# Optimization experiments

Hardware: AMD Instinct MI355X
Metric: run time of the kernel (lower is better)

Reference implementation:

```python
import jax, jax.numpy as jnp
import numpy as np

DIM = 256
NUM_HEADS = 8
HEAD_DIM = DIM // NUM_HEADS
SCALE = 1.0 / DIM ** 0.5  # NOTE: source scales by 1/sqrt(dim), not 1/sqrt(head_dim)


def setup_inputs() -> dict:
    key = jax.random.key(0)
    k_x, k_wqkv, k_wout = jax.random.split(key, 3)
    x = jax.random.normal(k_x, (4, 2048, DIM), dtype=jnp.float32)
    # xavier_uniform for Linear(dim, 3*dim): limit = sqrt(6/(fan_in+fan_out))
    lim_qkv = float(np.sqrt(6.0 / (DIM + 3 * DIM)))
    w_qkv = jax.random.uniform(k_wqkv, (3 * DIM, DIM), minval=-lim_qkv, maxval=lim_qkv, dtype=jnp.float32)
    b_qkv = jnp.zeros((3 * DIM,), dtype=jnp.float32)
    lim_out = float(np.sqrt(6.0 / (DIM + DIM)))
    w_out = jax.random.uniform(k_wout, (DIM, DIM), minval=-lim_out, maxval=lim_out, dtype=jnp.float32)
    b_out = jnp.zeros((DIM,), dtype=jnp.float32)
    return {"x": x, "w_qkv": w_qkv, "b_qkv": b_qkv, "w_out": w_out, "b_out": b_out}


def reference(x, w_qkv, b_qkv, w_out, b_out):
    B, N, C = x.shape
    H, D = NUM_HEADS, C // NUM_HEADS
    qkv = x @ w_qkv.T + b_qkv                       # [B, N, 3C]
    qkv = qkv.reshape(B, N, 3, H, D)
    q = qkv[:, :, 0].transpose(0, 2, 1, 3)          # [B, H, N, D]
    k = qkv[:, :, 1].transpose(0, 2, 1, 3)
    v = qkv[:, :, 2].transpose(0, 2, 1, 3)
    attn = jnp.einsum("bhnd,bhmd->bhnm", q, k) * SCALE  # [B, H, N, N]
    attn = jax.nn.softmax(attn, axis=-1)
    z = jnp.einsum("bhnm,bhmd->bhnd", attn, v)      # [B, H, N, D]
    z = z.transpose(0, 2, 1, 3).reshape(B, N, C)
    return z @ w_out.T + b_out
```

## Files before the change

### kernel.cpp

```cpp
#include <hip/hip_runtime.h>


#define SEQ 2048
#define BATCH 4
#define NHEADS 8
#define HDIM 32
#define DIMC 256
#define SCALE_LOG2E 0.09016844005556021f

typedef __attribute__((ext_vector_type(8))) short short8;
typedef __attribute__((ext_vector_type(4))) float f32x4;

union BF8 { unsigned u[4]; short8 s8; };

__device__ __forceinline__ unsigned pk2bf(float a, float b) {
    union { float f; unsigned u; } ua, ub;
    ua.f = a; ub.f = b;
    return __builtin_amdgcn_perm(ub.u + 0x8000u, ua.u + 0x8000u, 0x07060302u);
}
__device__ __forceinline__ short f2bf(float a) {
    union { float f; unsigned u; } x; x.f = a;
    return (short)((x.u + 0x8000u) >> 16);
}

#define NX (BATCH * SEQ * DIMC)
#define NQW (3 * DIMC * DIMC)
#define NOW (DIMC * DIMC)

__global__ __launch_bounds__(256) void cvt_bf16(const float* __restrict__ x,
                                                const float* __restrict__ wq,
                                                const float* __restrict__ wo,
                                                short* __restrict__ xb,
                                                short* __restrict__ wqb,
                                                short* __restrict__ wob) {
    int i = (blockIdx.x * 256 + threadIdx.x) * 4;
    const float* src;
    short* dst;
    int off;
    if (i < NX) { src = x; dst = xb; off = i; }
    else if (i < NX + NQW) { src = wq; dst = wqb; off = i - NX; }
    else { src = wo; dst = wob; off = i - NX - NQW; }
    float4 v = *(const float4*)&src[off];
    uint2 p;
    p.x = pk2bf(v.x, v.y);
    p.y = pk2bf(v.z, v.w);
    *(uint2*)&dst[off] = p;
}

__global__ __launch_bounds__(256) void qkv_mfma(const short* __restrict__ Xb,
                                                const short* __restrict__ Wb,
                                                const float* __restrict__ bias,
                                                short* __restrict__ Q,
                                                short* __restrict__ Kd,
                                                short* __restrict__ V) {
    __shared__ __align__(16) union SM {
        struct { short A[128][72]; short B[64][72]; } ab;
        short CQ[128][72];
        short CV[64][136];
    } sm;

    const int m0 = blockIdx.y * 128, bx = blockIdx.x;
    const int n0 = bx * 64;
    const int tid = threadIdx.x;
    const int w = tid >> 6, lane = tid & 63;
    const int m = lane & 15, g = lane >> 4;
    const int wr = w >> 1, wc = w & 1;

    const int arow = tid >> 1, acol = (tid & 1) * 32;
    const int brow = tid >> 2, bcol = (tid & 3) * 16;

    f32x4 acc[4][2] = {};

    const short* ap = Xb + (size_t)(m0 + arow) * DIMC + acol;
    const short* bp = Wb + (size_t)(n0 + brow) * DIMC + bcol;

    short8 pa[4], pb[2];
#pragma unroll
    for (int i = 0; i < 4; i++) pa[i] = *(const short8*)(ap + i * 8);
#pragma unroll
    for (int i = 0; i < 2; i++) pb[i] = *(const short8*)(bp + i * 8);

    for (int kt = 0; kt < DIMC; kt += 64) {
        __syncthreads();
#pragma unroll
        for (int i = 0; i < 4; i++) *(short8*)&sm.ab.A[arow][acol + i * 8] = pa[i];
#pragma unroll
        for (int i = 0; i < 2; i++) *(short8*)&sm.ab.B[brow][bcol + i * 8] = pb[i];
        __syncthreads();
        if (kt + 64 < DIMC) {
#pragma unroll
            for (int i = 0; i < 4; i++) pa[i] = *(const short8*)(ap + kt + 64 + i * 8);
#pragma unroll
            for (int i = 0; i < 2; i++) pb[i] = *(const short8*)(bp + kt + 64 + i * 8);
        }
#pragma unroll
        for (int kk = 0; kk < 2; kk++) {
            short8 af[4], bf[2];
#pragma unroll
            for (int mt = 0; mt < 4; mt++)
                af[mt] = *(const short8*)&sm.ab.A[wr * 64 + mt * 16 + m][kk * 32 + g * 8];
#pragma unroll
            for (int nt = 0; nt < 2; nt++)
                bf[nt] = *(const short8*)&sm.ab.B[wc * 32 + nt * 16 + m][kk * 32 + g * 8];
#pragma unroll
            for (int mt = 0; mt < 4; mt++)
#pragma unroll
                for (int nt = 0; nt < 2; nt++)
                    acc[mt][nt] = __builtin_amdgcn_mfma_f32_16x16x32_bf16(af[mt], bf[nt], acc[mt][nt], 0, 0, 0);
        }
    }

    const int which = bx >> 2;
    const int h0 = (bx & 3) * 2;
    const int bidx = blockIdx.y >> 4;
    const int ntok0 = (blockIdx.y & 15) * 128;
    float bv[2];
#pragma unroll
    for (int nt = 0; nt < 2; nt++) bv[nt] = bias[n0 + wc * 32 + nt * 16 + m];

    __syncthreads();
    if (which != 2) {
        const float qs = (which == 0) ? SCALE_LOG2E : 1.0f;
#pragma unroll
        for (int mt = 0; mt < 4; mt++)
#pragma unroll
            for (int nt = 0; nt < 2; nt++)
#pragma unroll
                for (int r = 0; r < 4; r++)
                    sm.CQ[wr * 64 + mt * 16 + g * 4 + r][wc * 32 + nt * 16 + m] =
                        f2bf((acc[mt][nt][r] + bv[nt]) * qs);
        __syncthreads();
        short* dst = (which == 0) ? Q : Kd;
        const int tok = tid >> 1, d0 = (tid & 1) * 16;
#pragma unroll
        for (int hh = 0; hh < 2; hh++) {
            size_t o = ((size_t)((bidx * NHEADS + h0 + hh) * SEQ) + ntok0 + tok) * HDIM + d0;
            *(short8*)&dst[o] = *(const short8*)&sm.CQ[tok][hh * 32 + d0];
            *(short8*)&dst[o + 8] = *(const short8*)&sm.CQ[tok][hh * 32 + d0 + 8];
        }
    } else {
#pragma unroll
        for (int mt = 0; mt < 4; mt++)
#pragma unroll
            for (int nt = 0; nt < 2; nt++) {
                uint2 p;
                p.x = pk2bf(acc[mt][nt][0] + bv[nt], acc[mt][nt][1] + bv[nt]);
                p.y = pk2bf(acc[mt][nt][2] + bv[nt], acc[mt][nt][3] + bv[nt]);
                *(uint2*)&sm.CV[wc * 32 + nt * 16 + m][wr * 64 + mt * 16 + g * 4] = p;
            }
        __syncthreads();
        const int col = tid >> 2, t0 = (tid & 3) * 32;
        const int hh = col >> 5, d = col & 31;
        size_t o = ((size_t)((bidx * NHEADS + h0 + hh) * HDIM) + d) * SEQ + ntok0 + t0;
#pragma unroll
        for (int c2 = 0; c2 < 4; c2++)
            *(short8*)&V[o + c2 * 8] = *(const short8*)&sm.CV[col][t0 + c2 * 8];
    }
}

__global__ __launch_bounds__(256, 2) void attn_tile(const short* __restrict__ Q,
                                                    const short* __restrict__ K,
                                                    const short* __restrict__ V,
                                                    short* __restrict__ Zb) {
    __shared__ __align__(16) union SM {
        struct { short Ks[2][128][40]; short Vs[2][32][136]; } kv;
        struct { float O[4][64][36]; float L[4][64]; } ep;
    } sm;

    const int bh = blockIdx.y;
    const int b = bh >> 3, h = bh & 7;
    const int q0 = blockIdx.x * 128;
    const short* qb = Q + (size_t)bh * SEQ * HDIM;
    const short* kb = K + (size_t)bh * SEQ * HDIM;
    const short* vb = V + (size_t)bh * HDIM * SEQ;
    const int tid = threadIdx.x;
    const int w = tid >> 6, lane = tid & 63;
    const int m = lane & 15, g = lane >> 4;

    short8 qfr[8];
#pragma unroll
    for (int qt = 0; qt < 8; qt++)
        qfr[qt] = *(const short8*)(qb + (size_t)(q0 + qt * 16 + m) * HDIM + g * 8);

    const int krow = tid >> 1, kcol = (tid & 1) * 16;
    const int rl = krow & 31;
    const int lrow = (krow & ~31) | (((rl >> 2) & 1) << 4) | ((rl >> 3) << 2) | (rl & 3);
    const int vrow = tid >> 3, vcol = (tid & 7) * 16;

    f32x4 o[8][2] = {};
    f32x4 ol[8] = {};
    const short8 ones = {0x3F80, 0x3F80, 0x3F80, 0x3F80, 0x3F80, 0x3F80, 0x3F80, 0x3F80};

    short8 k0a = *(const short8*)(kb + (size_t)krow * HDIM + kcol);
    short8 k0b = *(const short8*)(kb + (size_t)krow * HDIM + kcol + 8);
    short8 v0a = *(const short8*)(vb + (size_t)vrow * SEQ + vcol);
    short8 v0b = *(const short8*)(vb + (size_t)vrow * SEQ + vcol + 8);
    *(short8*)&sm.kv.Ks[0][lrow][kcol] = k0a;
    *(short8*)&sm.kv.Ks[0][lrow][kcol + 8] = k0b;
    *(short8*)&sm.kv.Vs[0][vrow][vcol] = v0a;
    *(short8*)&sm.kv.Vs[0][vrow][vcol + 8] = v0b;
    __syncthreads();

    for (int it = 0; it < SEQ / 128; ++it) {
        const int buf = it & 1;
        if (it < SEQ / 128 - 1) {
            const int kn = (it + 1) * 128;
            k0a = *(const short8*)(kb + (size_t)(kn + krow) * HDIM + kcol);
            k0b = *(const short8*)(kb + (size_t)(kn + krow) * HDIM + kcol + 8);
            v0a = *(const short8*)(vb + (size_t)vrow * SEQ + kn + vcol);
            v0b = *(const short8*)(vb + (size_t)vrow * SEQ + kn + vcol + 8);
        }

        short8 kf0 = *(const short8*)&sm.kv.Ks[buf][w * 32 + m][g * 8];
        short8 kf1 = *(const short8*)&sm.kv.Ks[buf][w * 32 + 16 + m][g * 8];
        short8 vf0 = *(const short8*)&sm.kv.Vs[buf][m][w * 32 + g * 8];
        short8 vf1 = *(const short8*)&sm.kv.Vs[buf][16 + m][w * 32 + g * 8];

#pragma unroll
        for (int qt = 0; qt < 8; qt++) {
            f32x4 z4 = {0.f, 0.f, 0.f, 0.f};
            f32x4 st0 = __builtin_amdgcn_mfma_f32_16x16x32_bf16(kf0, qfr[qt], z4, 0, 0, 0);
            f32x4 st1 = __builtin_amdgcn_mfma_f32_16x16x32_bf16(kf1, qfr[qt], z4, 0, 0, 0);
            BF8 a;
            a.u[0] = pk2bf(__builtin_amdgcn_exp2f(st0[0]), __builtin_amdgcn_exp2f(st0[1]));
            a.u[1] = pk2bf(__builtin_amdgcn_exp2f(st0[2]), __builtin_amdgcn_exp2f(st0[3]));
            a.u[2] = pk2bf(__builtin_amdgcn_exp2f(st1[0]), __builtin_amdgcn_exp2f(st1[1]));
            a.u[3] = pk2bf(__builtin_amdgcn_exp2f(st1[2]), __builtin_amdgcn_exp2f(st1[3]));
            o[qt][0] = __builtin_amdgcn_mfma_f32_16x16x32_bf16(a.s8, vf0, o[qt][0], 0, 0, 0);
            o[qt][1] = __builtin_amdgcn_mfma_f32_16x16x32_bf16(a.s8, vf1, o[qt][1], 0, 0, 0);
            ol[qt] = __builtin_amdgcn_mfma_f32_16x16x32_bf16(a.s8, ones, ol[qt], 0, 0, 0);
        }

        if (it < SEQ / 128 - 1) {
            const int nb = buf ^ 1;
            *(short8*)&sm.kv.Ks[nb][lrow][kcol] = k0a;
            *(short8*)&sm.kv.Ks[nb][lrow][kcol + 8] = k0b;
            *(short8*)&sm.kv.Vs[nb][vrow][vcol] = v0a;
            *(short8*)&sm.kv.Vs[nb][vrow][vcol + 8] = v0b;
        }
        __syncthreads();
    }

#pragma unroll
    for (int ph = 0; ph < 2; ph++) {
        if (ph) __syncthreads();
#pragma unroll
        for (int qt = 0; qt < 4; qt++) {
            const int qq = ph * 4 + qt;
#pragma unroll
            for (int dh = 0; dh < 2; dh++)
#pragma unroll
                for (int r = 0; r < 4; r++)
                    sm.ep.O[w][qt * 16 + g * 4 + r][dh * 16 + m] = o[qq][dh][r];
            if (m == 0)
#pragma unroll
                for (int r = 0; r < 4; r++)
                    sm.ep.L[w][qt * 16 + g * 4 + r] = ol[qq][r];
        }
        __syncthreads();

        const int ql = tid >> 2, d0 = (tid & 3) * 8;
        float lt = sm.ep.L[0][ql] + sm.ep.L[1][ql] + sm.ep.L[2][ql] + sm.ep.L[3][ql];
        float inv = __builtin_amdgcn_rcpf(lt);
        float sv[8];
#pragma unroll
        for (int j = 0; j < 8; j++)
            sv[j] = sm.ep.O[0][ql][d0 + j] + sm.ep.O[1][ql][d0 + j] +
                    sm.ep.O[2][ql][d0 + j] + sm.ep.O[3][ql][d0 + j];
        BF8 pz;
#pragma unroll
        for (int j = 0; j < 4; j++)
            pz.u[j] = pk2bf(sv[2 * j] * inv, sv[2 * j + 1] * inv);
        *(short8*)&Zb[(size_t)(b * SEQ + q0 + ph * 64 + ql) * DIMC + h * HDIM + d0] = pz.s8;
    }
}

__global__ __launch_bounds__(256) void out_mfma(const short* __restrict__ A,
                                                const short* __restrict__ Wb,
                                                const float* __restrict__ bias,
                                                float* __restrict__ C) {
    __shared__ __align__(16) short As[64][72];
    __shared__ __align__(16) short Bs[64][72];
    const int m0 = blockIdx.y * 64, n0 = blockIdx.x * 64;
    const int tid = threadIdx.x;
    const int w = tid >> 6, lane = tid & 63;
    const int m = lane & 15, g = lane >> 4;
    const int srow = tid >> 2, scol = (tid & 3) * 16;

    f32x4 acc[4] = {};

    const short* ap = A + (size_t)(m0 + srow) * DIMC + scol;
    const short* bp = Wb + (size_t)(n0 + srow) * DIMC + scol;

    short8 pa[2], pb[2];
#pragma unroll
    for (int i = 0; i < 2; i++) {
        pa[i] = *(const short8*)(ap + i * 8);
        pb[i] = *(const short8*)(bp + i * 8);
    }

    for (int kt = 0; kt < DIMC; kt += 64) {
        __syncthreads();
#pragma unroll
        for (int i = 0; i < 2; i++) {
            *(short8*)&As[srow][scol + i * 8] = pa[i];
            *(short8*)&Bs[srow][scol + i * 8] = pb[i];
        }
        __syncthreads();
        if (kt + 64 < DIMC) {
#pragma unroll
            for (int i = 0; i < 2; i++) {
                pa[i] = *(const short8*)(ap + kt + 64 + i * 8);
                pb[i] = *(const short8*)(bp + kt + 64 + i * 8);
            }
        }
#pragma unroll
        for (int kk = 0; kk < 2; kk++) {
            short8 af = *(const short8*)&As[w * 16 + m][kk * 32 + g * 8];
#pragma unroll
            for (int nt = 0; nt < 4; nt++) {
                short8 bf = *(const short8*)&Bs[nt * 16 + m][kk * 32 + g * 8];
                acc[nt] = __builtin_amdgcn_mfma_f32_16x16x32_bf16(af, bf, acc[nt], 0, 0, 0);
            }
        }
    }

    float bv[4];
#pragma unroll
    for (int nt = 0; nt < 4; nt++) bv[nt] = bias[n0 + nt * 16 + m];
#pragma unroll
    for (int nt = 0; nt < 4; nt++)
#pragma unroll
        for (int r = 0; r < 4; r++)
            C[(size_t)(m0 + w * 16 + g * 4 + r) * DIMC + n0 + nt * 16 + m] = acc[nt][r] + bv[nt];
}

extern "C" void kernel_launch(void* const* d_in, const int* in_sizes, int n_in,
                              void* d_out, int out_size, void* d_ws, size_t ws_size,
                              hipStream_t stream) {
    const float* x     = (const float*)d_in[0];
    const float* w_qkv = (const float*)d_in[1];
    const float* b_qkv = (const float*)d_in[2];
    const float* w_out = (const float*)d_in[3];
    const float* b_out = (const float*)d_in[4];
    float* out = (float*)d_out;

    const size_t HSZ = (size_t)BATCH * NHEADS * SEQ * HDIM;
    short* xb  = (short*)d_ws;
    short* wqb = xb + NX;
    short* wob = wqb + NQW;
    short* qw  = wob + NOW;
    short* kw  = qw + HSZ;
    short* vw  = kw + HSZ;
    short* zb  = vw + HSZ;

    cvt_bf16<<<(NX + NQW + NOW) / 1024, 256, 0, stream>>>(x, w_qkv, w_out, xb, wqb, wob);
    qkv_mfma<<<dim3(12, 64), 256, 0, stream>>>(xb, wqb, b_qkv, qw, kw, vw);
    attn_tile<<<dim3(16, 32), 256, 0, stream>>>(qw, kw, vw, zb);
    out_mfma<<<dim3(4, 128), 256, 0, stream>>>(zb, wob, b_out, out);
}
```

Measured before the change: 111.3 us.

## Split attention tile across eight waves with two query groups per block

```diff
diff --git a/kernel.cpp b/kernel.cpp
--- a/kernel.cpp
+++ b/kernel.cpp
@@ -158,13 +158,13 @@
     }
 }
 
-__global__ __launch_bounds__(256, 2) void attn_tile(const short* __restrict__ Q,
+__global__ __launch_bounds__(512, 4) void attn_tile(const short* __restrict__ Q,
                                                     const short* __restrict__ K,
                                                     const short* __restrict__ V,
                                                     short* __restrict__ Zb) {
     __shared__ __align__(16) union SM {
         struct { short Ks[2][128][40]; short Vs[2][32][136]; } kv;
-        struct { float O[4][64][36]; float L[4][64]; } ep;
+        struct { float O[4][128][36]; float L[4][128]; } ep;
     } sm;
 
     const int bh = blockIdx.y;
@@ -176,48 +176,43 @@
     const int tid = threadIdx.x;
     const int w = tid >> 6, lane = tid & 63;
     const int m = lane & 15, g = lane >> 4;
-
-    short8 qfr[8];
-#pragma unroll
-    for (int qt = 0; qt < 8; qt++)
-        qfr[qt] = *(const short8*)(qb + (size_t)(q0 + qt * 16 + m) * HDIM + g * 8);
-
-    const int krow = tid >> 1, kcol = (tid & 1) * 16;
+    const int wq = w >> 2, wk = w & 3;
+
+    short8 qfr[4];
+#pragma unroll
+    for (int qt = 0; qt < 4; qt++)
+        qfr[qt] = *(const short8*)(qb + (size_t)(q0 + wq * 64 + qt * 16 + m) * HDIM + g * 8);
+
+    const int krow = tid >> 2, kc8 = (tid & 3) * 8;
     const int rl = krow & 31;
     const int lrow = (krow & ~31) | (((rl >> 2) & 1) << 4) | ((rl >> 3) << 2) | (rl & 3);
-    const int vrow = tid >> 3, vcol = (tid & 7) * 16;
-
-    f32x4 o[8][2] = {};
-    f32x4 ol[8] = {};
+    const int vrow = tid >> 4, vc8 = (tid & 15) * 8;
+
+    f32x4 o[4][2] = {};
+    f32x4 ol[4] = {};
     const short8 ones = {0x3F80, 0x3F80, 0x3F80, 0x3F80, 0x3F80, 0x3F80, 0x3F80, 0x3F80};
 
-    short8 k0a = *(const short8*)(kb + (size_t)krow * HDIM + kcol);
-    short8 k0b = *(const short8*)(kb + (size_t)krow * HDIM + kcol + 8);
-    short8 v0a = *(const short8*)(vb + (size_t)vrow * SEQ + vcol);
-    short8 v0b = *(const short8*)(vb + (size_t)vrow * SEQ + vcol + 8);
-    *(short8*)&sm.kv.Ks[0][lrow][kcol] = k0a;
-    *(short8*)&sm.kv.Ks[0][lrow][kcol + 8] = k0b;
-    *(short8*)&sm.kv.Vs[0][vrow][vcol] = v0a;
-    *(short8*)&sm.kv.Vs[0][vrow][vcol + 8] = v0b;
+    short8 kst = *(const short8*)(kb + (size_t)krow * HDIM + kc8);
+    short8 vst = *(const short8*)(vb + (size_t)vrow * SEQ + vc8);
+    *(short8*)&sm.kv.Ks[0][lrow][kc8] = kst;
+    *(short8*)&sm.kv.Vs[0][vrow][vc8] = vst;
     __syncthreads();
 
     for (int it = 0; it < SEQ / 128; ++it) {
         const int buf = it & 1;
         if (it < SEQ / 128 - 1) {
             const int kn = (it + 1) * 128;
-            k0a = *(const short8*)(kb + (size_t)(kn + krow) * HDIM + kcol);
-            k0b = *(const short8*)(kb + (size_t)(kn + krow) * HDIM + kcol + 8);
-            v0a = *(const short8*)(vb + (size_t)vrow * SEQ + kn + vcol);
-            v0b = *(const short8*)(vb + (size_t)vrow * SEQ + kn + vcol + 8);
-        }
-
-        short8 kf0 = *(const short8*)&sm.kv.Ks[buf][w * 32 + m][g * 8];
-        short8 kf1 = *(const short8*)&sm.kv.Ks[buf][w * 32 + 16 + m][g * 8];
-        short8 vf0 = *(const short8*)&sm.kv.Vs[buf][m][w * 32 + g * 8];
-        short8 vf1 = *(const short8*)&sm.kv.Vs[buf][16 + m][w * 32 + g * 8];
-
-#pragma unroll
-        for (int qt = 0; qt < 8; qt++) {
+            kst = *(const short8*)(kb + (size_t)(kn + krow) * HDIM + kc8);
+            vst = *(const short8*)(vb + (size_t)vrow * SEQ + kn + vc8);
+        }
+
+        short8 kf0 = *(const short8*)&sm.kv.Ks[buf][wk * 32 + m][g * 8];
+        short8 kf1 = *(const short8*)&sm.kv.Ks[buf][wk * 32 + 16 + m][g * 8];
+        short8 vf0 = *(const short8*)&sm.kv.Vs[buf][m][wk * 32 + g * 8];
+        short8 vf1 = *(const short8*)&sm.kv.Vs[buf][16 + m][wk * 32 + g * 8];
+
+#pragma unroll
+        for (int qt = 0; qt < 4; qt++) {
             f32x4 z4 = {0.f, 0.f, 0.f, 0.f};
             f32x4 st0 = __builtin_amdgcn_mfma_f32_16x16x32_bf16(kf0, qfr[qt], z4, 0, 0, 0);
             f32x4 st1 = __builtin_amdgcn_mfma_f32_16x16x32_bf16(kf1, qfr[qt], z4, 0, 0, 0);
@@ -233,46 +228,39 @@
 
         if (it < SEQ / 128 - 1) {
             const int nb = buf ^ 1;
-            *(short8*)&sm.kv.Ks[nb][lrow][kcol] = k0a;
-            *(short8*)&sm.kv.Ks[nb][lrow][kcol + 8] = k0b;
-            *(short8*)&sm.kv.Vs[nb][vrow][vcol] = v0a;
-            *(short8*)&sm.kv.Vs[nb][vrow][vcol + 8] = v0b;
-        }
-        __syncthreads();
-    }
-
-#pragma unroll
-    for (int ph = 0; ph < 2; ph++) {
-        if (ph) __syncthreads();
-#pragma unroll
-        for (int qt = 0; qt < 4; qt++) {
-            const int qq = ph * 4 + qt;
-#pragma unroll
-            for (int dh = 0; dh < 2; dh++)
-#pragma unroll
-                for (int r = 0; r < 4; r++)
-                    sm.ep.O[w][qt * 16 + g * 4 + r][dh * 16 + m] = o[qq][dh][r];
-            if (m == 0)
-#pragma unroll
-                for (int r = 0; r < 4; r++)
-                    sm.ep.L[w][qt * 16 + g * 4 + r] = ol[qq][r];
-        }
-        __syncthreads();
-
-        const int ql = tid >> 2, d0 = (tid & 3) * 8;
-        float lt = sm.ep.L[0][ql] + sm.ep.L[1][ql] + sm.ep.L[2][ql] + sm.ep.L[3][ql];
-        float inv = __builtin_amdgcn_rcpf(lt);
-        float sv[8];
-#pragma unroll
-        for (int j = 0; j < 8; j++)
-            sv[j] = sm.ep.O[0][ql][d0 + j] + sm.ep.O[1][ql][d0 + j] +
-                    sm.ep.O[2][ql][d0 + j] + sm.ep.O[3][ql][d0 + j];
-        BF8 pz;
-#pragma unroll
-        for (int j = 0; j < 4; j++)
-            pz.u[j] = pk2bf(sv[2 * j] * inv, sv[2 * j + 1] * inv);
-        *(short8*)&Zb[(size_t)(b * SEQ + q0 + ph * 64 + ql) * DIMC + h * HDIM + d0] = pz.s8;
-    }
+            *(short8*)&sm.kv.Ks[nb][lrow][kc8] = kst;
+            *(short8*)&sm.kv.Vs[nb][vrow][vc8] = vst;
+        }
+        __syncthreads();
+    }
+
+#pragma unroll
+    for (int qt = 0; qt < 4; qt++) {
+#pragma unroll
+        for (int dh = 0; dh < 2; dh++)
+#pragma unroll
+            for (int r = 0; r < 4; r++)
+                sm.ep.O[wk][wq * 64 + qt * 16 + g * 4 + r][dh * 16 + m] = o[qt][dh][r];
+        if (m == 0)
+#pragma unroll
+            for (int r = 0; r < 4; r++)
+                sm.ep.L[wk][wq * 64 + qt * 16 + g * 4 + r] = ol[qt][r];
+    }
+    __syncthreads();
+
+    const int ql = tid >> 2, d0 = (tid & 3) * 8;
+    float lt = sm.ep.L[0][ql] + sm.ep.L[1][ql] + sm.ep.L[2][ql] + sm.ep.L[3][ql];
+    float inv = __builtin_amdgcn_rcpf(lt);
+    float sv[8];
+#pragma unroll
+    for (int j = 0; j < 8; j++)
+        sv[j] = sm.ep.O[0][ql][d0 + j] + sm.ep.O[1][ql][d0 + j] +
+                sm.ep.O[2][ql][d0 + j] + sm.ep.O[3][ql][d0 + j];
+    BF8 pz;
+#pragma unroll
+    for (int j = 0; j < 4; j++)
+        pz.u[j] = pk2bf(sv[2 * j] * inv, sv[2 * j + 1] * inv);
+    *(short8*)&Zb[(size_t)(b * SEQ + q0 + ql) * DIMC + h * HDIM + d0] = pz.s8;
 }
 
 __global__ __launch_bounds__(256) void out_mfma(const short* __restrict__ A,
@@ -356,6 +344,6 @@
 
     cvt_bf16<<<(NX + NQW + NOW) / 1024, 256, 0, stream>>>(x, w_qkv, w_out, xb, wqb, wob);
     qkv_mfma<<<dim3(12, 64), 256, 0, stream>>>(xb, wqb, b_qkv, qw, kw, vw);
-    attn_tile<<<dim3(16, 32), 256, 0, stream>>>(qw, kw, vw, zb);
+    attn_tile<<<dim3(16, 32), 512, 0, stream>>>(qw, kw, vw, zb);
     out_mfma<<<dim3(4, 128), 256, 0, stream>>>(zb, wob, b_out, out);
 }
```

New measurement: 112.9 us. Within noise of the previous version (+1.4%).
